# Optimization experiments

Measured on AMD Instinct MI355X. Metric: run time of the kernel, lower is better.

Reference implementation:

```python
import jax, jax.numpy as jnp
import numpy as np

B, N, E = 128, 4096, 262144  # batch, num_vertices, num_edges


def setup_inputs() -> dict:
    key = jax.random.key(0)
    k1, k2, k3, k4, k5 = jax.random.split(key, 5)
    x = jax.random.normal(k1, (B, N), dtype=jnp.float32)
    error = jax.random.normal(k2, (B, N), dtype=jnp.float32)
    w = jax.random.normal(k3, (N, N), dtype=jnp.float32) * 0.02  # dense weight matrix, masked by adj in orig
    src = jax.random.randint(k4, (E,), 0, N)
    tgt = jax.random.randint(k5, (E,), 0, N)
    edge_index = jnp.stack([src, tgt]).astype(jnp.int32)  # [2, E]
    return {"x": x, "error": error, "w": w, "edge_index": edge_index}


def reference(x, error, w, edge_index):
    # Activation f = tanh, dfdx = 1 - tanh^2 (set_activation convention).
    src, tgt = edge_index[0], edge_index[1]
    w_e = w[src, tgt]  # per-edge weight gather, [E]

    # --- PredictionMessagePassing (flow='target_to_source', aggr='add') ---
    # message: f(x_j) * weight with x_j = x[tgt]; aggregated at src nodes.
    fx_t = jnp.tanh(x[:, tgt])                          # [B, E]
    mu = jnp.zeros_like(x).at[:, src].add(fx_t * w_e)   # scatter-add -> [B, N]

    # --- GradientMessagePassing (flow='source_to_target', aggr='add') ---
    # message: dfdx(x_i) * error_j * weight with x_i = x[tgt], error_j = error[src];
    # aggregated at tgt nodes; update: error - aggr_out.
    dfdx_t = 1.0 - fx_t * fx_t                          # [B, E]
    aggr = jnp.zeros_like(x).at[:, tgt].add(dfdx_t * error[:, src] * w_e)
    dEdx = error - aggr                                 # [B, N]

    return mu, dEdx
```

## Files before the change

### kernel.cpp

```cpp
#include <hip/hip_runtime.h>
#include <hip/hip_fp16.h>
#include <math.h>

#define B    128
#define NV   4096
#define NE   262144
#define CAP  192
#define KSC  256
#define EPB  1024
#define NS   8192


__device__ inline float2 h2f(unsigned u) {
    __half2 h;
    *reinterpret_cast<unsigned*>(&h) = u;
    return __half22float2(h);
}
__device__ inline float wlo(unsigned r) {
    return __half2float(__ushort_as_half((unsigned short)(r & 0xffffu)));
}

__global__ __launch_bounds__(256)
void k_count(const int* __restrict__ ei, unsigned* __restrict__ hist) {
    __shared__ unsigned hc[NS];
    const int t = threadIdx.x, blk = blockIdx.x;
#pragma unroll
    for (int i = 0; i < NS / 256; ++i) hc[t + 256 * i] = 0u;
    __syncthreads();
    const int base = blk * EPB + t;
#pragma unroll
    for (int i = 0; i < 4; ++i) {
        const int e = base + 256 * i;
        atomicAdd(&hc[ei[e]], 1u);
        atomicAdd(&hc[4096 + ei[NE + e]], 1u);
    }
    __syncthreads();
    unsigned* hrow = hist + (size_t)blk * NS;
#pragma unroll
    for (int i = 0; i < NS / 256; ++i) hrow[t + 256 * i] = hc[t + 256 * i];
}

__global__ __launch_bounds__(256)
void k_mid(const float* __restrict__ x, const float* __restrict__ err,
           float* __restrict__ T_t, float* __restrict__ err_t,
           ushort* __restrict__ Th, ushort* __restrict__ Eh,
           const unsigned* __restrict__ hist, unsigned* __restrict__ off,
           unsigned* __restrict__ count) {
    __shared__ float tile0[32][33];
    __shared__ float tile1[32][33];
    const int t = threadIdx.x, blk = blockIdx.x;

    if (blk < 512) {
        const int n0 = (blk & 127) * 32;
        const int b0 = (blk >> 7) * 32;
        const int a = t & 31, c0 = t >> 5;
#pragma unroll
        for (int r = 0; r < 4; ++r) {
            int c = c0 + 8 * r;
            int gi = (b0 + c) * NV + (n0 + a);
            tile0[c][a] = tanhf(x[gi]);
            tile1[c][a] = err[gi];
        }
        __syncthreads();
#pragma unroll
        for (int r = 0; r < 4; ++r) {
            int c = c0 + 8 * r;
            int go = (n0 + c) * B + (b0 + a);
            float tv = tile0[a][c];
            float ev = tile1[a][c];
            T_t[go]   = tv;
            err_t[go] = ev;
            Th[go] = __half_as_ushort(__float2half_rn(tv));
            Eh[go] = __half_as_ushort(__float2half_rn(ev));
        }
    } else {
        const int n    = (blk - 512) * 4 + (t >> 6);
        const int lane = t & 63;
        unsigned h[4];
#pragma unroll
        for (int i = 0; i < 4; ++i)
            h[i] = hist[(size_t)(4 * lane + i) * NS + n];
        unsigned s = h[0] + h[1] + h[2] + h[3];
        unsigned inc = s;
#pragma unroll
        for (int d = 1; d < 64; d <<= 1) {
            unsigned v = __shfl_up(inc, d, 64);
            if (lane >= d) inc += v;
        }
        unsigned base = inc - s;
        unsigned p = 0;
#pragma unroll
        for (int i = 0; i < 4; ++i) {
            off[(size_t)(4 * lane + i) * NS + n] = base + p;
            p += h[i];
        }
        if (lane == 63) count[n] = inc;
    }
}

__global__ __launch_bounds__(256)
void k_place(const int* __restrict__ ei, const float* __restrict__ w,
             const unsigned* __restrict__ off,
             unsigned* __restrict__ es, unsigned* __restrict__ et) {
    __shared__ unsigned slot[NS];
    const int t = threadIdx.x, blk = blockIdx.x;
    const unsigned* orow = off + (size_t)blk * NS;
#pragma unroll
    for (int i = 0; i < NS / 256; ++i) slot[t + 256 * i] = orow[t + 256 * i];
    const int base = blk * EPB + t;
    int sn[4], tn[4];
    unsigned wh[4];
#pragma unroll
    for (int i = 0; i < 4; ++i) {
        const int e = base + 256 * i;
        sn[i] = ei[e];
        tn[i] = ei[NE + e];
    }
#pragma unroll
    for (int i = 0; i < 4; ++i)
        wh[i] = (unsigned)__half_as_ushort(
            __float2half_rn(w[(size_t)sn[i] * NV + tn[i]]));
    __syncthreads();
    unsigned p[4], q[4];
#pragma unroll
    for (int i = 0; i < 4; ++i) {
        p[i] = atomicAdd(&slot[sn[i]], 1u);
        q[i] = atomicAdd(&slot[4096 + tn[i]], 1u);
    }
#pragma unroll
    for (int i = 0; i < 4; ++i) {
        if (p[i] < CAP) es[sn[i] * CAP + p[i]] = ((unsigned)tn[i] << 16) | wh[i];
        if (q[i] < CAP) et[tn[i] * CAP + q[i]] = ((unsigned)sn[i] << 16) | wh[i];
    }
}

__global__ __launch_bounds__(64)
void k_proc(const unsigned* __restrict__ count,
            const unsigned* __restrict__ es, const unsigned* __restrict__ et,
            const float* __restrict__ T_t, const float* __restrict__ err_t,
            const unsigned* __restrict__ Th2, const unsigned* __restrict__ Eh2,
            float* __restrict__ out) {
    const int raw    = blockIdx.x;
    const bool is_mu = raw < NV;
    const int b2     = is_mu ? raw : raw - NV;
    const int node   = (b2 & 7) * (NV / 8) + (b2 >> 3);
    int n_e = (int)count[is_mu ? node : NV + node];
    if (n_e > CAP) n_e = CAP;
    const unsigned* ed  = (is_mu ? es : et) + node * CAP;
    const int4*     ed4 = (const int4*)ed;
    const unsigned* srcH = is_mu ? Th2 : Eh2;
    const int lane = threadIdx.x;

    float2 a0 = make_float2(0.f, 0.f), a1 = make_float2(0.f, 0.f);
    float2 a2 = make_float2(0.f, 0.f), a3 = make_float2(0.f, 0.f);
    float2 a4 = make_float2(0.f, 0.f), a5 = make_float2(0.f, 0.f);
    float2 a6 = make_float2(0.f, 0.f), a7 = make_float2(0.f, 0.f);
    int k = 0;
    for (; k + 8 <= n_e; k += 8) {
        int4 mA = ed4[(k >> 2) + 0];
        int4 mB = ed4[(k >> 2) + 1];
        const unsigned r0 = (unsigned)mA.x, r1 = (unsigned)mA.y;
        const unsigned r2 = (unsigned)mA.z, r3 = (unsigned)mA.w;
        const unsigned r4 = (unsigned)mB.x, r5 = (unsigned)mB.y;
        const unsigned r6 = (unsigned)mB.z, r7 = (unsigned)mB.w;
        unsigned g0 = srcH[(r0 >> 16) * (B / 2) + lane];
        unsigned g1 = srcH[(r1 >> 16) * (B / 2) + lane];
        unsigned g2 = srcH[(r2 >> 16) * (B / 2) + lane];
        unsigned g3 = srcH[(r3 >> 16) * (B / 2) + lane];
        unsigned g4 = srcH[(r4 >> 16) * (B / 2) + lane];
        unsigned g5 = srcH[(r5 >> 16) * (B / 2) + lane];
        unsigned g6 = srcH[(r6 >> 16) * (B / 2) + lane];
        unsigned g7 = srcH[(r7 >> 16) * (B / 2) + lane];
        float w0 = wlo(r0), w1 = wlo(r1), w2 = wlo(r2), w3 = wlo(r3);
        float w4 = wlo(r4), w5 = wlo(r5), w6 = wlo(r6), w7 = wlo(r7);
        float2 t0 = h2f(g0), t1 = h2f(g1), t2 = h2f(g2), t3 = h2f(g3);
        float2 t4 = h2f(g4), t5 = h2f(g5), t6 = h2f(g6), t7 = h2f(g7);
        a0.x += t0.x * w0; a0.y += t0.y * w0;
        a1.x += t1.x * w1; a1.y += t1.y * w1;
        a2.x += t2.x * w2; a2.y += t2.y * w2;
        a3.x += t3.x * w3; a3.y += t3.y * w3;
        a4.x += t4.x * w4; a4.y += t4.y * w4;
        a5.x += t5.x * w5; a5.y += t5.y * w5;
        a6.x += t6.x * w6; a6.y += t6.y * w6;
        a7.x += t7.x * w7; a7.y += t7.y * w7;
    }
    for (; k < n_e; ++k) {
        unsigned r = ed[k];
        unsigned g = srcH[(r >> 16) * (B / 2) + lane];
        float wv = wlo(r);
        float2 tv = h2f(g);
        a0.x += tv.x * wv; a0.y += tv.y * wv;
    }
    a0.x += a1.x; a0.y += a1.y;  a2.x += a3.x; a2.y += a3.y;
    a4.x += a5.x; a4.y += a5.y;  a6.x += a7.x; a6.y += a7.y;
    a0.x += a2.x; a0.y += a2.y;  a4.x += a6.x; a4.y += a6.y;
    float2 acc = make_float2(a0.x + a4.x, a0.y + a4.y);

    const int b0 = 2 * lane;
    if (is_mu) {
        out[(size_t)b0 * NV + node]       = acc.x;
        out[(size_t)(b0 + 1) * NV + node] = acc.y;
    } else {
        const int oi = node * (B / 2) + lane;
        float2 th = ((const float2*)T_t)[oi];
        float2 er = ((const float2*)err_t)[oi];
        float* o2 = out + (size_t)B * NV;
        o2[(size_t)b0 * NV + node]       = er.x - (1.f - th.x * th.x) * acc.x;
        o2[(size_t)(b0 + 1) * NV + node] = er.y - (1.f - th.y * th.y) * acc.y;
    }
}

extern "C" void kernel_launch(void* const* d_in, const int* in_sizes, int n_in,
                              void* d_out, int out_size, void* d_ws, size_t ws_size,
                              hipStream_t stream) {
    const float* x   = (const float*)d_in[0];
    const float* err = (const float*)d_in[1];
    const float* w   = (const float*)d_in[2];
    const int*   ei  = (const int*)d_in[3];
    float* out = (float*)d_out;

    const int NB = NV * B;
    float*    T_t   = (float*)d_ws;
    float*    err_t = T_t + NB;
    ushort*   Th    = (ushort*)(err_t + NB);
    ushort*   Eh    = Th + NB;
    unsigned* hist  = (unsigned*)(Eh + NB);
    unsigned* off   = hist + (size_t)KSC * NS;
    unsigned* count = off + (size_t)KSC * NS;
    unsigned* es    = count + NS;
    unsigned* et    = es + (size_t)NV * CAP;

    k_count<<<KSC, 256, 0, stream>>>(ei, hist);
    k_mid<<<512 + NS / 4, 256, 0, stream>>>(x, err, T_t, err_t, Th, Eh,
                                            hist, off, count);
    k_place<<<KSC, 256, 0, stream>>>(ei, w, off, es, et);
    k_proc<<<2 * NV, 64, 0, stream>>>(count, es, et, T_t, err_t,
                                      (const unsigned*)Th, (const unsigned*)Eh, out);
}
```

Measured before the change: 152.5 us.

## Merge histogram count into transpose kernel and use shared-memory column scan

The edge histogram counting now runs in the same launch as the x/error transpose, so the two independent jobs overlap. The prefix scan is moved into its own kernel that stages 64 columns of the histogram in shared memory and scans them with 4-way segmented shuffles. The number of scatter blocks is halved to 128 with 2048 edges each, which shrinks the histogram and offset arrays. The cost is a separate scan launch and fewer, heavier blocks in the count and place phases.

After: 135.2 us. 1.13x faster.

```diff
diff --git a/kernel.cpp b/kernel.cpp
--- a/kernel.cpp
+++ b/kernel.cpp
@@ -6,9 +6,10 @@
 #define NV   4096
 #define NE   262144
 #define CAP  192
-#define KSC  256
-#define EPB  1024
+#define KSC  128
+#define EPB  2048
 #define NS   8192
+#define SCOLS 64
 
 
 __device__ inline float2 h2f(unsigned u) {
@@ -21,36 +22,17 @@
 }
 
 __global__ __launch_bounds__(256)
-void k_count(const int* __restrict__ ei, unsigned* __restrict__ hist) {
-    __shared__ unsigned hc[NS];
+void k_tc(const float* __restrict__ x, const float* __restrict__ err,
+          const int* __restrict__ ei,
+          float* __restrict__ T_t, float* __restrict__ err_t,
+          ushort* __restrict__ Th, ushort* __restrict__ Eh,
+          unsigned* __restrict__ hist) {
+    __shared__ unsigned shm[NS];
     const int t = threadIdx.x, blk = blockIdx.x;
-#pragma unroll
-    for (int i = 0; i < NS / 256; ++i) hc[t + 256 * i] = 0u;
-    __syncthreads();
-    const int base = blk * EPB + t;
-#pragma unroll
-    for (int i = 0; i < 4; ++i) {
-        const int e = base + 256 * i;
-        atomicAdd(&hc[ei[e]], 1u);
-        atomicAdd(&hc[4096 + ei[NE + e]], 1u);
-    }
-    __syncthreads();
-    unsigned* hrow = hist + (size_t)blk * NS;
-#pragma unroll
-    for (int i = 0; i < NS / 256; ++i) hrow[t + 256 * i] = hc[t + 256 * i];
-}
-
-__global__ __launch_bounds__(256)
-void k_mid(const float* __restrict__ x, const float* __restrict__ err,
-           float* __restrict__ T_t, float* __restrict__ err_t,
-           ushort* __restrict__ Th, ushort* __restrict__ Eh,
-           const unsigned* __restrict__ hist, unsigned* __restrict__ off,
-           unsigned* __restrict__ count) {
-    __shared__ float tile0[32][33];
-    __shared__ float tile1[32][33];
-    const int t = threadIdx.x, blk = blockIdx.x;
 
     if (blk < 512) {
+        float* tile0 = (float*)shm;
+        float* tile1 = tile0 + 1056;
         const int n0 = (blk & 127) * 32;
         const int b0 = (blk >> 7) * 32;
         const int a = t & 31, c0 = t >> 5;
@@ -58,43 +40,73 @@
         for (int r = 0; r < 4; ++r) {
             int c = c0 + 8 * r;
             int gi = (b0 + c) * NV + (n0 + a);
-            tile0[c][a] = tanhf(x[gi]);
-            tile1[c][a] = err[gi];
+            tile0[c * 33 + a] = tanhf(x[gi]);
+            tile1[c * 33 + a] = err[gi];
         }
         __syncthreads();
 #pragma unroll
         for (int r = 0; r < 4; ++r) {
             int c = c0 + 8 * r;
             int go = (n0 + c) * B + (b0 + a);
-            float tv = tile0[a][c];
-            float ev = tile1[a][c];
+            float tv = tile0[a * 33 + c];
+            float ev = tile1[a * 33 + c];
             T_t[go]   = tv;
             err_t[go] = ev;
             Th[go] = __half_as_ushort(__float2half_rn(tv));
             Eh[go] = __half_as_ushort(__float2half_rn(ev));
         }
     } else {
-        const int n    = (blk - 512) * 4 + (t >> 6);
-        const int lane = t & 63;
-        unsigned h[4];
-#pragma unroll
-        for (int i = 0; i < 4; ++i)
-            h[i] = hist[(size_t)(4 * lane + i) * NS + n];
-        unsigned s = h[0] + h[1] + h[2] + h[3];
-        unsigned inc = s;
-#pragma unroll
-        for (int d = 1; d < 64; d <<= 1) {
-            unsigned v = __shfl_up(inc, d, 64);
-            if (lane >= d) inc += v;
+        const int blk2 = blk - 512;
+#pragma unroll
+        for (int i = 0; i < NS / 256; ++i) shm[t + 256 * i] = 0u;
+        __syncthreads();
+        const int base = blk2 * EPB + t;
+#pragma unroll
+        for (int i = 0; i < 8; ++i) {
+            const int e = base + 256 * i;
+            atomicAdd(&shm[ei[e]], 1u);
+            atomicAdd(&shm[4096 + ei[NE + e]], 1u);
         }
-        unsigned base = inc - s;
-        unsigned p = 0;
-#pragma unroll
-        for (int i = 0; i < 4; ++i) {
-            off[(size_t)(4 * lane + i) * NS + n] = base + p;
-            p += h[i];
-        }
-        if (lane == 63) count[n] = inc;
+        __syncthreads();
+        unsigned* hrow = hist + (size_t)blk2 * NS;
+#pragma unroll
+        for (int i = 0; i < NS / 256; ++i) hrow[t + 256 * i] = shm[t + 256 * i];
+    }
+}
+
+__global__ __launch_bounds__(256)
+void k_scan(const unsigned* __restrict__ hist, unsigned* __restrict__ off,
+            unsigned* __restrict__ count) {
+    __shared__ unsigned p[KSC * SCOLS];
+    const int t  = threadIdx.x;
+    const int n0 = blockIdx.x * SCOLS;
+#pragma unroll
+    for (int i = 0; i < (KSC * SCOLS) / 256; ++i) {
+        int l = t + 256 * i;
+        p[l] = hist[(size_t)(l >> 6) * NS + n0 + (l & 63)];
+    }
+    __syncthreads();
+    const int col = t >> 2, seg = t & 3;
+    unsigned s = 0;
+#pragma unroll
+    for (int j = 0; j < KSC / 4; ++j) s += p[(seg * (KSC / 4) + j) * SCOLS + col];
+    unsigned inc = s;
+    unsigned v1 = __shfl_up(inc, 1, 4); if (seg >= 1) inc += v1;
+    unsigned v2 = __shfl_up(inc, 2, 4); if (seg >= 2) inc += v2;
+    unsigned run = inc - s;
+    if (seg == 3) count[n0 + col] = inc;
+#pragma unroll
+    for (int j = 0; j < KSC / 4; ++j) {
+        int idx = (seg * (KSC / 4) + j) * SCOLS + col;
+        unsigned old = p[idx];
+        p[idx] = run;
+        run += old;
+    }
+    __syncthreads();
+#pragma unroll
+    for (int i = 0; i < (KSC * SCOLS) / 256; ++i) {
+        int l = t + 256 * i;
+        off[(size_t)(l >> 6) * NS + n0 + (l & 63)] = p[l];
     }
 }
 
@@ -108,29 +120,29 @@
 #pragma unroll
     for (int i = 0; i < NS / 256; ++i) slot[t + 256 * i] = orow[t + 256 * i];
     const int base = blk * EPB + t;
-    int sn[4], tn[4];
-    unsigned wh[4];
-#pragma unroll
-    for (int i = 0; i < 4; ++i) {
+    int sn[8], tn[8];
+    unsigned wh[8];
+#pragma unroll
+    for (int i = 0; i < 8; ++i) {
         const int e = base + 256 * i;
         sn[i] = ei[e];
         tn[i] = ei[NE + e];
     }
 #pragma unroll
-    for (int i = 0; i < 4; ++i)
+    for (int i = 0; i < 8; ++i)
         wh[i] = (unsigned)__half_as_ushort(
             __float2half_rn(w[(size_t)sn[i] * NV + tn[i]]));
     __syncthreads();
-    unsigned p[4], q[4];
-#pragma unroll
-    for (int i = 0; i < 4; ++i) {
-        p[i] = atomicAdd(&slot[sn[i]], 1u);
-        q[i] = atomicAdd(&slot[4096 + tn[i]], 1u);
-    }
-#pragma unroll
-    for (int i = 0; i < 4; ++i) {
-        if (p[i] < CAP) es[sn[i] * CAP + p[i]] = ((unsigned)tn[i] << 16) | wh[i];
-        if (q[i] < CAP) et[tn[i] * CAP + q[i]] = ((unsigned)sn[i] << 16) | wh[i];
+    unsigned pp[8], qq[8];
+#pragma unroll
+    for (int i = 0; i < 8; ++i) {
+        pp[i] = atomicAdd(&slot[sn[i]], 1u);
+        qq[i] = atomicAdd(&slot[4096 + tn[i]], 1u);
+    }
+#pragma unroll
+    for (int i = 0; i < 8; ++i) {
+        if (pp[i] < CAP) es[sn[i] * CAP + pp[i]] = ((unsigned)tn[i] << 16) | wh[i];
+        if (qq[i] < CAP) et[tn[i] * CAP + qq[i]] = ((unsigned)sn[i] << 16) | wh[i];
     }
 }
 
@@ -230,9 +242,8 @@
     unsigned* es    = count + NS;
     unsigned* et    = es + (size_t)NV * CAP;
 
-    k_count<<<KSC, 256, 0, stream>>>(ei, hist);
-    k_mid<<<512 + NS / 4, 256, 0, stream>>>(x, err, T_t, err_t, Th, Eh,
-                                            hist, off, count);
+    k_tc<<<512 + KSC, 256, 0, stream>>>(x, err, ei, T_t, err_t, Th, Eh, hist);
+    k_scan<<<NS / SCOLS, 256, 0, stream>>>(hist, off, count);
     k_place<<<KSC, 256, 0, stream>>>(ei, w, off, es, et);
     k_proc<<<2 * NV, 64, 0, stream>>>(count, es, et, T_t, err_t,
                                       (const unsigned*)Th, (const unsigned*)Eh, out);
```
